# Optimization experiments

Measured on AMD Instinct MI355X. Metric: run time of the kernel, lower is better.

Reference implementation:

```python
import jax, jax.numpy as jnp
import numpy as np

V, E, H, D, DFF, NB, C, B, T = 32000, 512, 256, 512, 2048, 4, 16, 32, 512
PAD, BOS, EOS = 0, 1, 2


def positional_encoding(t, d):
    pos = jnp.arange(t, dtype=jnp.float32)[:, None]
    i = jnp.arange(0, d, 2, dtype=jnp.float32)
    div = jnp.exp(-(jnp.log(10000.0)) * i / d)
    pe = jnp.zeros((t, d), jnp.float32)
    pe = pe.at[:, 0::2].set(jnp.sin(pos * div))
    pe = pe.at[:, 1::2].set(jnp.cos(pos * div))
    return pe


def layernorm(x, g, b, eps=1e-5):
    mu = jnp.mean(x, -1, keepdims=True)
    var = jnp.mean((x - mu) ** 2, -1, keepdims=True)
    return (x - mu) * jax.lax.rsqrt(var + eps) * g + b


def gru_dir(xs, w_ih, w_hh, b_ih, b_hh, reverse):
    # xs: (B,T,E); precompute input projections for all t (one big GEMM)
    gi = jnp.einsum('bte,ge->btg', xs, w_ih) + b_ih  # (B,T,3H)
    h0 = jnp.zeros((xs.shape[0], H), xs.dtype)

    def step(h, gi_t):
        gh = h @ w_hh.T + b_hh
        i_r, i_z, i_n = jnp.split(gi_t, 3, -1)
        h_r, h_z, h_n = jnp.split(gh, 3, -1)
        r = jax.nn.sigmoid(i_r + h_r)
        z = jax.nn.sigmoid(i_z + h_z)
        n = jnp.tanh(i_n + r * h_n)
        h_new = (1.0 - z) * n + z * h
        return h_new, h_new

    _, hs = jax.lax.scan(step, h0, jnp.swapaxes(gi, 0, 1), reverse=reverse)
    return jnp.swapaxes(hs, 0, 1)  # (B,T,H)


def forward(x, y, embed_W, w_ih_f, w_hh_f, b_ih_f, b_hh_f, w_ih_b, w_hh_b, b_ih_b, b_hh_b,
            ff_w1, ff_b1, ff_w2, ff_b2, ln_g, ln_b, fc_w, fc_b, trans):
    h = embed_W[x]                                   # (B,T,E)
    h = h + positional_encoding(h.shape[1], E)[None]
    hf = gru_dir(h, w_ih_f, w_hh_f, b_ih_f, b_hh_f, False)
    hb = gru_dir(h, w_ih_b, w_hh_b, b_ih_b, b_hh_b, True)
    h = jnp.concatenate([hf, hb], -1)                # (B,T,D)
    for i in range(NB):                              # FeedForward blocks (residual + LN)
        ff = jax.nn.relu(h @ ff_w1[i] + ff_b1[i]) @ ff_w2[i] + ff_b2[i]
        h = layernorm(h + ff, ln_g[i], ln_b[i])
    logits = h @ fc_w + fc_b                         # (B,T,C) emissions

    # --- CRF viterbi decode ---
    mask = (y != PAD)                                # (B,T) bool
    emit = jnp.swapaxes(logits, 0, 1)                # (T,B,C)
    m = jnp.swapaxes(mask, 0, 1)                     # (T,B)
    score0 = trans[BOS][None] + emit[0]              # (B,C)

    def vstep(score, inp):
        e_t, m_t = inp                               # (B,C), (B,)
        cand = score[:, :, None] + trans[None] + e_t[:, None, :]  # (B,prev,cur)
        new = jnp.max(cand, axis=1)
        bp = jnp.argmax(cand, axis=1)                # (B,C)
        new = jnp.where(m_t[:, None], new, score)
        return new, bp

    final, bps = jax.lax.scan(vstep, score0, (emit[1:], m[1:]))  # bps: (T-1,B,C)
    final = final + trans[:, EOS][None]
    best_score = jnp.max(final, -1)                  # (B,)
    last_tag = jnp.argmax(final, -1)                 # (B,)

    def back(tag, inp):
        bp_t, m_t = inp
        prev = jnp.take_along_axis(bp_t, tag[:, None], axis=1)[:, 0]
        prev = jnp.where(m_t, prev, tag)
        return prev, tag

    first_tag, rest = jax.lax.scan(back, last_tag, (bps, m[1:]), reverse=True)
    path = jnp.swapaxes(jnp.concatenate([first_tag[None], rest], 0), 0, 1)  # (B,T)
    return best_score, path


def setup_inputs():
    key = jax.random.key(0)
    ks = jax.random.split(key, 16)
    nrm = lambda k, sh, sc: jax.random.normal(k, sh, jnp.float32) * sc
    s = 1.0 / float(np.sqrt(H))
    inp = {}
    inp['x'] = jax.random.randint(ks[0], (B, T), 1, V)
    inp['y'] = jax.random.randint(ks[1], (B, T), 0, 13) + 3  # in [3,16): no pad/bos/eos
    inp['embed_W'] = nrm(ks[2], (V, E), 0.02)
    inp['w_ih_f'] = nrm(ks[3], (3 * H, E), s); inp['w_hh_f'] = nrm(ks[4], (3 * H, H), s)
    inp['b_ih_f'] = nrm(ks[5], (3 * H,), s); inp['b_hh_f'] = nrm(ks[6], (3 * H,), s)
    inp['w_ih_b'] = nrm(ks[7], (3 * H, E), s); inp['w_hh_b'] = nrm(ks[8], (3 * H, H), s)
    inp['b_ih_b'] = nrm(ks[9], (3 * H,), s); inp['b_hh_b'] = nrm(ks[10], (3 * H,), s)
    inp['ff_w1'] = nrm(ks[11], (NB, D, DFF), 1.0 / float(np.sqrt(D)))
    inp['ff_b1'] = jnp.zeros((NB, DFF), jnp.float32)
    inp['ff_w2'] = nrm(ks[12], (NB, DFF, D), 1.0 / float(np.sqrt(DFF)))
    inp['ff_b2'] = jnp.zeros((NB, D), jnp.float32)
    inp['ln_g'] = jnp.ones((NB, D), jnp.float32); inp['ln_b'] = jnp.zeros((NB, D), jnp.float32)
    inp['fc_w'] = nrm(ks[13], (D, C), 1.0 / float(np.sqrt(D)))
    inp['fc_b'] = jnp.zeros((C,), jnp.float32)
    inp['trans'] = nrm(ks[14], (C, C), 0.1)
    return inp


def reference(x, y, embed_W, w_ih_f, w_hh_f, b_ih_f, b_hh_f, w_ih_b, w_hh_b, b_ih_b, b_hh_b,
              ff_w1, ff_b1, ff_w2, ff_b2, ln_g, ln_b, fc_w, fc_b, trans):
    return forward(x, y, embed_W, w_ih_f, w_hh_f, b_ih_f, b_hh_f, w_ih_b, w_hh_b, b_ih_b, b_hh_b,
                   ff_w1, ff_b1, ff_w2, ff_b2, ln_g, ln_b, fc_w, fc_b, trans)
```

## Files before the change

### kernel.cpp

```cpp
#include <hip/hip_runtime.h>

#define DEV __device__ __forceinline__

using short8 = __attribute__((ext_vector_type(8))) short;
using f32x4  = __attribute__((ext_vector_type(4))) float;

DEV float b2f(short s) {
  union { unsigned u; float f; } c;
  c.u = ((unsigned)(unsigned short)s) << 16;
  return c.f;
}
DEV short f2b(float f) {
  union { float f; unsigned u; } c; c.f = f;
  unsigned u = c.u + 0x7fffu + ((c.u >> 16) & 1u);
  return (short)(u >> 16);
}
DEV float fast_sigmoid(float x) {
  return __builtin_amdgcn_rcpf(1.f + __expf(-x));
}
DEV float fast_tanh(float x) {
  return 1.f - 2.f * __builtin_amdgcn_rcpf(1.f + __expf(2.f * x));
}
DEV void async_ld16(const void* g, void* lds) {
  __builtin_amdgcn_global_load_lds(
      (const __attribute__((address_space(1))) void*)(unsigned long long)g,
      (__attribute__((address_space(3))) void*)(unsigned)(unsigned long long)lds,
      16, 0, 0);
}

__global__ __launch_bounds__(256) void k_cvt2(const float* __restrict__ a, const float* __restrict__ b,
                                              short* __restrict__ oa, short* __restrict__ ob) {
  int blk = blockIdx.x;
  const float* in; short* out; int base;
  if (blk < 384) { in = a; out = oa; base = blk; }
  else           { in = b; out = ob; base = blk - 384; }
  int i = base * 256 + threadIdx.x;
  f32x4 v = *(const f32x4*)(in + (size_t)i * 4);
  short4 o;
#pragma unroll
  for (int j = 0; j < 4; j++) ((short*)&o)[j] = f2b(v[j]);
  *(short4*)(out + (size_t)i * 4) = o;
}

__global__ __launch_bounds__(256) void k_w8(const float* __restrict__ wf,
                                            const float* __restrict__ wb,
                                            long* __restrict__ out) {
  int flat = blockIdx.x * 256 + threadIdx.x;
  int lane = flat & 63;
  int r1 = flat >> 6;
  int kb = r1 & 7;
  int r2 = r1 >> 3;
  int g = r2 % 3;
  int r3 = r2 / 3;
  int v = r3 & 15;
  int d = r3 >> 4;
  const float* w = d ? wb : wf;
  int row = g * 256 + v * 16 + (lane & 15);
  int k0 = kb * 32 + (lane >> 4) * 8;
  const float* p = w + (size_t)row * 256 + k0;
  f32x4 f0 = *(const f32x4*)(p);
  f32x4 f1 = *(const f32x4*)(p + 4);
  int u0 = __builtin_amdgcn_cvt_pk_fp8_f32(f0[0], f0[1], 0, false);
  u0 = __builtin_amdgcn_cvt_pk_fp8_f32(f0[2], f0[3], u0, true);
  int u1 = __builtin_amdgcn_cvt_pk_fp8_f32(f1[0], f1[1], 0, false);
  u1 = __builtin_amdgcn_cvt_pk_fp8_f32(f1[2], f1[3], u1, true);
  out[flat] = ((long)(unsigned)u1 << 32) | (unsigned)u0;
}

__global__ __launch_bounds__(256) void k_embed(const int* __restrict__ x,
                                               const float* __restrict__ W,
                                               short* __restrict__ h0) {
  int flat = blockIdx.x * 256 + threadIdx.x;
  int row  = flat >> 6;
  int e0   = (flat & 63) << 3;
  int tok  = x[row];
  int t    = row & 511;
  const float* wp = W + (size_t)tok * 512 + e0;
  float v[8];
  *(f32x4*)v       = *(const f32x4*)(wp);
  *(f32x4*)(v + 4) = *(const f32x4*)(wp + 4);
  short8 o;
#pragma unroll
  for (int i = 0; i < 8; i += 2) {
    float f = expf(-9.210340371976184f * (float)(e0 + i) * (1.f / 512.f));
    float ang = (float)t * f;
    o[i]     = f2b(v[i]     + sinf(ang));
    o[i + 1] = f2b(v[i + 1] + cosf(ang));
  }
  *(short8*)(h0 + (size_t)flat * 8) = o;
}

__global__ __launch_bounds__(256) void k_transcvt(const float* __restrict__ in0,
                                                  short* __restrict__ out0, int R, int C) {
  __shared__ float tile[32][33];
  int mat = blockIdx.x >> 10;
  const float* in = in0 + (size_t)mat * 1048576;
  short* out = out0 + (size_t)mat * 1048576;
  int blk = blockIdx.x & 1023;
  int ct = C >> 5;
  int bc = blk % ct, br = blk / ct;
  int r0 = br << 5, c0 = bc << 5;
  for (int i = threadIdx.x; i < 1024; i += 256) {
    int r = i >> 5, c = i & 31;
    tile[r][c] = in[(size_t)(r0 + r) * C + c0 + c];
  }
  __syncthreads();
  for (int i = threadIdx.x; i < 1024; i += 256) {
    int c = i >> 5, r = i & 31;
    out[(size_t)(c0 + c) * R + r0 + r] = f2b(tile[r][c]);
  }
}

template <int MODE>
__global__ __launch_bounds__(256) void k_gemm(const short* __restrict__ A,
    const short* __restrict__ B, const float* __restrict__ bias,
    float* __restrict__ Cf, short* __restrict__ Cb, int M, int N, int K) {
  __shared__ short smA[8192];
  __shared__ short smB[8192];
  const int tid = threadIdx.x, lane = tid & 63, wave = tid >> 6;
  const int m15 = lane & 15, q8 = (lane >> 4) << 3;
  const int tn = N >> 7;
  const int bm = blockIdx.x / tn, bn = blockIdx.x % tn;
  const int wm = wave & 1, wn = wave >> 1;
  const f32x4 z4 = {0.f, 0.f, 0.f, 0.f};
  f32x4 acc[4][4];
#pragma unroll
  for (int i = 0; i < 4; i++)
#pragma unroll
    for (int j = 0; j < 4; j++) acc[i][j] = z4;

  for (int k0 = 0; k0 < K; k0 += 64) {
#pragma unroll
    for (int is = 0; is < 4; is++) {
      int c = is * 4 + wave;
      int mb = c & 7, kb = c >> 3;
      async_ld16(A + (size_t)(bm * 128 + mb * 16 + m15) * K + k0 + kb * 32 + q8, smA + c * 512);
      async_ld16(B + (size_t)(bn * 128 + mb * 16 + m15) * K + k0 + kb * 32 + q8, smB + c * 512);
    }
    __syncthreads();
#pragma unroll
    for (int kk = 0; kk < 2; kk++) {
      short8 af[4], bf[4];
#pragma unroll
      for (int i = 0; i < 4; i++)
        af[i] = *(const short8*)(smA + (kk * 8 + wm * 4 + i) * 512 + lane * 8);
#pragma unroll
      for (int j = 0; j < 4; j++)
        bf[j] = *(const short8*)(smB + (kk * 8 + wn * 4 + j) * 512 + lane * 8);
#pragma unroll
      for (int i = 0; i < 4; i++)
#pragma unroll
        for (int j = 0; j < 4; j++)
          acc[i][j] = __builtin_amdgcn_mfma_f32_16x16x32_bf16(af[i], bf[j], acc[i][j], 0, 0, 0);
    }
    __syncthreads();
  }
#pragma unroll
  for (int j = 0; j < 4; j++) {
    int col = bn * 128 + wn * 64 + j * 16 + m15;
    float bv = bias[col];
#pragma unroll
    for (int i = 0; i < 4; i++) {
      int row0 = bm * 128 + wm * 64 + i * 16 + ((lane >> 4) << 2);
#pragma unroll
      for (int r = 0; r < 4; r++) {
        float v = acc[i][j][r] + bv;
        int rr = row0 + r;
        if (MODE == 0) {
          Cf[(size_t)rr * N + col] = v;
        } else if (MODE == 1) {
          if (v < 0.f) v = 0.f;
          Cb[(size_t)rr * N + col] = f2b(v);
        } else {
          Cb[((size_t)((rr & 511) * 32 + (rr >> 9))) * 768 + col] = f2b(v);
        }
      }
    }
  }
}

__global__ __launch_bounds__(1024) void k_gru(
    const long* __restrict__ w8,
    const float* __restrict__ bhh_f, const float* __restrict__ bhh_b,
    const short* __restrict__ gi16_f, const short* __restrict__ gi16_b,
    short* __restrict__ hcat16) {
  __shared__ char  hb[2][4352];
  __shared__ float smG[16][200];
  const int blk = blockIdx.x;
  const int d = blk & 1, bg = blk >> 1;
  const int tid = threadIdx.x, lane = tid & 63, v = tid >> 6;
  const int m15 = lane & 15, quad = lane >> 4, q8 = quad * 8;
  const int col = v * 16 + m15;
  const int brow = quad;
  const float* bhh = d ? bhh_b : bhh_f;
  const short* gi  = d ? gi16_b : gi16_f;

  long Bf[3][8];
  {
    const long* wp = w8 + (size_t)(d * 16 + v) * 1536;
#pragma unroll
    for (int g = 0; g < 3; g++)
#pragma unroll
      for (int kb = 0; kb < 8; kb++)
        Bf[g][kb] = wp[(g * 8 + kb) * 64 + lane];
  }
  float bh[3];
#pragma unroll
  for (int g = 0; g < 3; g++) bh[g] = bhh[g * 256 + col];

  for (int i = tid; i < 2176; i += 1024) ((int*)hb)[i] = 0;

  const int t0 = d ? 511 : 0;
  const long gdelta = (long)(d ? -1 : 1) * 32 * 768;
  const long hdelta = (long)(d ? -1 : 1) * 32 * 512;
  const short* gp0 = gi + ((size_t)t0 * 32 + bg * 4 + brow) * 768 + col;
  const short* gp1 = gp0 + 256;
  const short* gp2 = gp0 + 512;
  short* hflush = hcat16 + ((size_t)t0 * 32 + bg * 4 + brow) * 512 + d * 256 + col;

  float gic0 = b2f(*gp0), gic1 = b2f(*gp1), gic2 = b2f(*gp2);
  gp0 += gdelta; gp1 += gdelta; gp2 += gdelta;
  float hprev = 0.f;
  unsigned obuf[4] = {0u, 0u, 0u, 0u};
  const f32x4 z4 = {0.f, 0.f, 0.f, 0.f};
  __syncthreads();

  for (int s = 0; s < 512; s++) {
    short n0 = 0, n1 = 0, n2 = 0;
    if (s < 511) {
      n0 = *gp0; n1 = *gp1; n2 = *gp2;
      gp0 += gdelta; gp1 += gdelta; gp2 += gdelta;
    }
    const char* hs = hb[s & 1];
    f32x4 acc0 = z4, acc1 = z4, acc2 = z4;
#pragma unroll
    for (int kb = 0; kb < 8; kb++) {
      long a = *(const long*)(hs + m15 * 272 + kb * 32 + q8);
      acc0 = __builtin_amdgcn_mfma_f32_16x16x32_fp8_fp8(a, Bf[0][kb], acc0, 0, 0, 0);
      acc1 = __builtin_amdgcn_mfma_f32_16x16x32_fp8_fp8(a, Bf[1][kb], acc1, 0, 0, 0);
      acc2 = __builtin_amdgcn_mfma_f32_16x16x32_fp8_fp8(a, Bf[2][kb], acc2, 0, 0, 0);
    }
    if (quad == 0) {
#pragma unroll
      for (int i = 0; i < 4; i++) {
        smG[v][i * 16 + m15]       = acc0[i];
        smG[v][64 + i * 16 + m15]  = acc1[i];
        smG[v][128 + i * 16 + m15] = acc2[i];
      }
    }
    float gr = smG[v][lane];
    float gz = smG[v][64 + lane];
    float gn = smG[v][128 + lane];
    float r = fast_sigmoid(gic0 + gr + bh[0]);
    float z = fast_sigmoid(gic1 + gz + bh[1]);
    float n = fast_tanh(gic2 + r * (gn + bh[2]));
    float h = (1.f - z) * n + z * hprev;
    hprev = h;
    int p8 = __builtin_amdgcn_cvt_pk_fp8_f32(h, h, 0, false);
    hb[(s + 1) & 1][brow * 272 + col] = (char)(p8 & 0xff);
    unsigned hb16 = (unsigned)(unsigned short)f2b(h);
    int idx = s & 7;
    if ((idx & 1) == 0) obuf[idx >> 1] = hb16;
    else                obuf[idx >> 1] |= hb16 << 16;
    if (idx == 7) {
      short* p = hflush;
#pragma unroll
      for (int k = 0; k < 8; k++) {
        *p = (short)(obuf[k >> 1] >> ((k & 1) * 16));
        p += hdelta;
      }
      hflush += 8 * hdelta;
    }
    gic0 = b2f(n0); gic1 = b2f(n1); gic2 = b2f(n2);
    __syncthreads();
  }
}

template <int FIRST>
__global__ __launch_bounds__(256) void k_ln(const float* __restrict__ hinf,
    const float* __restrict__ ff, const float* __restrict__ gw,
    const float* __restrict__ bw, float* __restrict__ hout, short* __restrict__ h16) {
  int row = blockIdx.x * 4 + (threadIdx.x >> 6);
  int lane = threadIdx.x & 63;
  size_t base = (size_t)row * 512 + lane * 8;
  f32x4 x0, x1;
  if (FIRST) {
    short8 hv = *(const short8*)(h16 + base);
#pragma unroll
    for (int i = 0; i < 4; i++) { x0[i] = b2f(hv[i]); x1[i] = b2f(hv[4 + i]); }
  } else {
    x0 = *(const f32x4*)(hinf + base);
    x1 = *(const f32x4*)(hinf + base + 4);
  }
  f32x4 y0 = *(const f32x4*)(ff + base);
  f32x4 y1 = *(const f32x4*)(ff + base + 4);
  x0 += y0; x1 += y1;
  float s = x0[0] + x0[1] + x0[2] + x0[3] + x1[0] + x1[1] + x1[2] + x1[3];
#pragma unroll
  for (int off = 32; off >= 1; off >>= 1) s += __shfl_xor(s, off);
  float mu = s * (1.f / 512.f);
  float vv = 0.f;
#pragma unroll
  for (int i = 0; i < 4; i++) { float d0 = x0[i] - mu, d1 = x1[i] - mu; vv += d0 * d0 + d1 * d1; }
#pragma unroll
  for (int off = 32; off >= 1; off >>= 1) vv += __shfl_xor(vv, off);
  float rs = rsqrtf(vv * (1.f / 512.f) + 1e-5f);
  int e = lane * 8;
  f32x4 g0 = *(const f32x4*)(gw + e), g1 = *(const f32x4*)(gw + e + 4);
  f32x4 bb0 = *(const f32x4*)(bw + e), bb1 = *(const f32x4*)(bw + e + 4);
  f32x4 o0, o1; short8 ob;
#pragma unroll
  for (int i = 0; i < 4; i++) {
    float a = (x0[i] - mu) * rs * g0[i] + bb0[i];
    float b = (x1[i] - mu) * rs * g1[i] + bb1[i];
    o0[i] = a; o1[i] = b; ob[i] = f2b(a); ob[4 + i] = f2b(b);
  }
  *(f32x4*)(hout + base) = o0;
  *(f32x4*)(hout + base + 4) = o1;
  *(short8*)(h16 + base) = ob;
}

__global__ __launch_bounds__(256) void k_fc(const float* __restrict__ h,
    const float* __restrict__ fcw, const float* __restrict__ bias,
    float* __restrict__ logits) {
  int row = blockIdx.x * 4 + (threadIdx.x >> 6);
  int lane = threadIdx.x & 63;
  int c = lane & 15, part = lane >> 4;
  const float* ph = h + (size_t)row * 512 + part * 128;
  const float* pw = fcw + (size_t)part * 128 * 16 + c;
  float acc = 0.f;
#pragma unroll 8
  for (int k = 0; k < 128; k += 4) {
    f32x4 hv = *(const f32x4*)(ph + k);
    acc += hv[0] * pw[(k) * 16] + hv[1] * pw[(k + 1) * 16]
         + hv[2] * pw[(k + 2) * 16] + hv[3] * pw[(k + 3) * 16];
  }
  acc += __shfl_xor(acc, 16);
  acc += __shfl_xor(acc, 32);
  if (part == 0) logits[(size_t)row * 16 + c] = acc + bias[c];
}

__global__ __launch_bounds__(64) void k_crf(const float* __restrict__ logits,
    const int* __restrict__ y, const float* __restrict__ trans,
    float* __restrict__ out) {
  __shared__ float tr[16][16];
  __shared__ unsigned char bp[511][16];
  int b = blockIdx.x, lane = threadIdx.x;
  for (int i = lane; i < 256; i += 64) tr[i >> 4][i & 15] = trans[i];
  __syncthreads();
  int cur = lane & 15;
  const float* lg = logits + (size_t)b * 16;
  const int* yb = y + b * 512;
  float score = tr[1][cur] + lg[cur];
  float e_next = lg[512 + cur];
  int y_next = yb[1];
  for (int t = 1; t < 512; t++) {
    float e = e_next; int ym = y_next;
    if (t < 511) { e_next = lg[(t + 1) * 512 + cur]; y_next = yb[t + 1]; }
    float best = -3.4e38f; int arg = 0;
#pragma unroll
    for (int p = 0; p < 16; p++) {
      float cand = __shfl(score, p) + tr[p][cur];
      if (cand > best) { best = cand; arg = p; }
    }
    if (lane < 16) bp[t - 1][cur] = (unsigned char)arg;
    float ns = best + e;
    if (ym == 0) ns = score;
    score = ns;
  }
  score += tr[cur][2];
  float best = -3.4e38f; int argb = 0;
#pragma unroll
  for (int p = 0; p < 16; p++) {
    float sp = __shfl(score, p);
    if (sp > best) { best = sp; argb = p; }
  }
  __syncthreads();
  if (lane == 0) {
    out[b] = best;
    float* po = out + 32 + (size_t)b * 512;
    int tag = argb;
    po[511] = (float)tag;
    for (int t = 511; t >= 1; t--) {
      int prev = bp[t - 1][tag];
      if (yb[t] == 0) prev = tag;
      po[t - 1] = (float)prev;
      tag = prev;
    }
  }
}

extern "C" void kernel_launch(void* const* d_in, const int* in_sizes, int n_in,
                              void* d_out, int out_size, void* d_ws, size_t ws_size,
                              hipStream_t stream) {
  const int*   x      = (const int*)d_in[0];
  const int*   y      = (const int*)d_in[1];
  const float* embedW = (const float*)d_in[2];
  const float* w_ih_f = (const float*)d_in[3];
  const float* w_hh_f = (const float*)d_in[4];
  const float* b_ih_f = (const float*)d_in[5];
  const float* b_hh_f = (const float*)d_in[6];
  const float* w_ih_b = (const float*)d_in[7];
  const float* w_hh_b = (const float*)d_in[8];
  const float* b_ih_b = (const float*)d_in[9];
  const float* b_hh_b = (const float*)d_in[10];
  const float* ff_w1  = (const float*)d_in[11];
  const float* ff_b1  = (const float*)d_in[12];
  const float* ff_w2  = (const float*)d_in[13];
  const float* ff_b2  = (const float*)d_in[14];
  const float* ln_g   = (const float*)d_in[15];
  const float* ln_b   = (const float*)d_in[16];
  const float* fc_w   = (const float*)d_in[17];
  const float* fc_b   = (const float*)d_in[18];
  const float* trans  = (const float*)d_in[19];
  float* out = (float*)d_out;

  char* ws = (char*)d_ws;
  short* h0     = (short*)(ws + 0);
  short* gi16_f = (short*)(ws + 16777216);
  short* gi16_b = (short*)(ws + 41943040);
  short* mid    = (short*)(ws + 16777216);
  float* ffout  = (float*)(ws + 83886080);
  short* wihf16 = (short*)(ws + 117440512);
  short* wihb16 = (short*)(ws + 118226944);
  long*  w8     = (long*) (ws + 119013376);
  short* w1t    = (short*)(ws + 119799808);
  short* w2t    = (short*)(ws + 128188416);
  short* hcat16 = (short*)(ws + 136577024);
  float* hres   = (float*)(ws + 153354240);
  float* logits = (float*)(ws + 186908672);

  k_embed<<<4096, 256, 0, stream>>>(x, embedW, h0);
  k_cvt2<<<768, 256, 0, stream>>>(w_ih_f, w_ih_b, wihf16, wihb16);
  k_w8<<<192, 256, 0, stream>>>(w_hh_f, w_hh_b, w8);
  k_transcvt<<<4096, 256, 0, stream>>>(ff_w1, w1t, 512, 2048);
  k_transcvt<<<4096, 256, 0, stream>>>(ff_w2, w2t, 2048, 512);

  k_gemm<2><<<768, 256, 0, stream>>>(h0, wihf16, b_ih_f, nullptr, gi16_f, 16384, 768, 512);
  k_gemm<2><<<768, 256, 0, stream>>>(h0, wihb16, b_ih_b, nullptr, gi16_b, 16384, 768, 512);

  k_gru<<<16, 1024, 0, stream>>>(w8, b_hh_f, b_hh_b, gi16_f, gi16_b, hcat16);

  for (int i = 0; i < 4; i++) {
    k_gemm<1><<<2048, 256, 0, stream>>>(hcat16, w1t + (size_t)i * 1048576, ff_b1 + i * 2048,
                                        nullptr, mid, 16384, 2048, 512);
    k_gemm<0><<<512, 256, 0, stream>>>(mid, w2t + (size_t)i * 1048576, ff_b2 + i * 512,
                                       ffout, nullptr, 16384, 512, 2048);
    if (i == 0)
      k_ln<1><<<4096, 256, 0, stream>>>(nullptr, ffout, ln_g, ln_b, hres, hcat16);
    else
      k_ln<0><<<4096, 256, 0, stream>>>(hres, ffout, ln_g + i * 512, ln_b + i * 512, hres, hcat16);
  }
  k_fc<<<4096, 256, 0, stream>>>(hres, fc_w, fc_b, logits);
  k_crf<<<32, 64, 0, stream>>>(logits, y, trans, out);
}
```

Baseline: 1.779 ms.

## Merge GRU input GEMMs and swizzle GRU hidden-state LDS layout for vector loads

The forward and backward input-projection GEMMs become one N=1536 GEMM that writes an interleaved gate buffer. This relies on the two bf16 weight copies sitting next to each other in the workspace, and a new bias2 argument selects the bias per half. In the serial GRU kernel, the fp8 hidden state is stored in a permuted, XOR-swizzled LDS layout. Each lane can then fetch all eight MFMA A fragments with four 128-bit loads instead of eight 64-bit loads, cutting LDS latency on the recurrent critical path. The bf16 output flush also moves to the top of the next step so its stores overlap that step's work.

```diff
diff --git a/kernel.cpp b/kernel.cpp
--- a/kernel.cpp
+++ b/kernel.cpp
@@ -4,6 +4,7 @@
 
 using short8 = __attribute__((ext_vector_type(8))) short;
 using f32x4  = __attribute__((ext_vector_type(4))) float;
+using i64x2  = __attribute__((ext_vector_type(2))) long;
 
 DEV float b2f(short s) {
   union { unsigned u; float f; } c;
@@ -114,6 +115,7 @@
 template <int MODE>
 __global__ __launch_bounds__(256) void k_gemm(const short* __restrict__ A,
     const short* __restrict__ B, const float* __restrict__ bias,
+    const float* __restrict__ bias2,
     float* __restrict__ Cf, short* __restrict__ Cb, int M, int N, int K) {
   __shared__ short smA[8192];
   __shared__ short smB[8192];
@@ -158,7 +160,9 @@
 #pragma unroll
   for (int j = 0; j < 4; j++) {
     int col = bn * 128 + wn * 64 + j * 16 + m15;
-    float bv = bias[col];
+    float bv;
+    if (MODE == 3) bv = (col < 768) ? bias[col] : bias2[col - 768];
+    else           bv = bias[col];
 #pragma unroll
     for (int i = 0; i < 4; i++) {
       int row0 = bm * 128 + wm * 64 + i * 16 + ((lane >> 4) << 2);
@@ -172,7 +176,7 @@
           if (v < 0.f) v = 0.f;
           Cb[(size_t)rr * N + col] = f2b(v);
         } else {
-          Cb[((size_t)((rr & 511) * 32 + (rr >> 9))) * 768 + col] = f2b(v);
+          Cb[((size_t)((rr & 511) * 32 + (rr >> 9))) * 1536 + col] = f2b(v);
         }
       }
     }
@@ -182,18 +186,17 @@
 __global__ __launch_bounds__(1024) void k_gru(
     const long* __restrict__ w8,
     const float* __restrict__ bhh_f, const float* __restrict__ bhh_b,
-    const short* __restrict__ gi16_f, const short* __restrict__ gi16_b,
+    const short* __restrict__ gi16,
     short* __restrict__ hcat16) {
-  __shared__ char  hb[2][4352];
+  __shared__ __align__(16) char hb[2][4096];
   __shared__ float smG[16][200];
   const int blk = blockIdx.x;
   const int d = blk & 1, bg = blk >> 1;
   const int tid = threadIdx.x, lane = tid & 63, v = tid >> 6;
-  const int m15 = lane & 15, quad = lane >> 4, q8 = quad * 8;
+  const int m15 = lane & 15, quad = lane >> 4;
   const int col = v * 16 + m15;
   const int brow = quad;
   const float* bhh = d ? bhh_b : bhh_f;
-  const short* gi  = d ? gi16_b : gi16_f;
 
   long Bf[3][8];
   {
@@ -208,12 +211,20 @@
 #pragma unroll
   for (int g = 0; g < 3; g++) bh[g] = bhh[g * 256 + col];
 
-  for (int i = tid; i < 2176; i += 1024) ((int*)hb)[i] = 0;
+  const int sw = (m15 & 3) << 4;
+  const int aof0 = m15 * 256 + ((quad * 64 +  0) ^ sw);
+  const int aof1 = m15 * 256 + ((quad * 64 + 16) ^ sw);
+  const int aof2 = m15 * 256 + ((quad * 64 + 32) ^ sw);
+  const int aof3 = m15 * 256 + ((quad * 64 + 48) ^ sw);
+  const int Lw = (((col >> 3) & 3) << 6) + ((col >> 5) << 3) + (col & 7);
+  const int wofs = brow * 256 + (Lw ^ (brow << 4));
+
+  for (int i = tid; i < 2048; i += 1024) ((int*)hb)[i] = 0;
 
   const int t0 = d ? 511 : 0;
-  const long gdelta = (long)(d ? -1 : 1) * 32 * 768;
+  const long gdelta = (long)(d ? -1 : 1) * 32 * 1536;
   const long hdelta = (long)(d ? -1 : 1) * 32 * 512;
-  const short* gp0 = gi + ((size_t)t0 * 32 + bg * 4 + brow) * 768 + col;
+  const short* gp0 = gi16 + ((size_t)t0 * 32 + bg * 4 + brow) * 1536 + d * 768 + col;
   const short* gp1 = gp0 + 256;
   const short* gp2 = gp0 + 512;
   short* hflush = hcat16 + ((size_t)t0 * 32 + bg * 4 + brow) * 512 + d * 256 + col;
@@ -226,19 +237,32 @@
   __syncthreads();
 
   for (int s = 0; s < 512; s++) {
+    if ((s & 7) == 0 && s) {
+      short* p = hflush;
+#pragma unroll
+      for (int k = 0; k < 8; k++) {
+        *p = (short)(obuf[k >> 1] >> ((k & 1) * 16));
+        p += hdelta;
+      }
+      hflush += 8 * hdelta;
+    }
     short n0 = 0, n1 = 0, n2 = 0;
     if (s < 511) {
       n0 = *gp0; n1 = *gp1; n2 = *gp2;
       gp0 += gdelta; gp1 += gdelta; gp2 += gdelta;
     }
     const char* hs = hb[s & 1];
+    i64x2 p0 = *(const i64x2*)(hs + aof0);
+    i64x2 p1 = *(const i64x2*)(hs + aof1);
+    i64x2 p2 = *(const i64x2*)(hs + aof2);
+    i64x2 p3 = *(const i64x2*)(hs + aof3);
+    long Af[8] = {p0[0], p0[1], p1[0], p1[1], p2[0], p2[1], p3[0], p3[1]};
     f32x4 acc0 = z4, acc1 = z4, acc2 = z4;
 #pragma unroll
     for (int kb = 0; kb < 8; kb++) {
-      long a = *(const long*)(hs + m15 * 272 + kb * 32 + q8);
-      acc0 = __builtin_amdgcn_mfma_f32_16x16x32_fp8_fp8(a, Bf[0][kb], acc0, 0, 0, 0);
-      acc1 = __builtin_amdgcn_mfma_f32_16x16x32_fp8_fp8(a, Bf[1][kb], acc1, 0, 0, 0);
-      acc2 = __builtin_amdgcn_mfma_f32_16x16x32_fp8_fp8(a, Bf[2][kb], acc2, 0, 0, 0);
+      acc0 = __builtin_amdgcn_mfma_f32_16x16x32_fp8_fp8(Af[kb], Bf[0][kb], acc0, 0, 0, 0);
+      acc1 = __builtin_amdgcn_mfma_f32_16x16x32_fp8_fp8(Af[kb], Bf[1][kb], acc1, 0, 0, 0);
+      acc2 = __builtin_amdgcn_mfma_f32_16x16x32_fp8_fp8(Af[kb], Bf[2][kb], acc2, 0, 0, 0);
     }
     if (quad == 0) {
 #pragma unroll
@@ -257,22 +281,21 @@
     float h = (1.f - z) * n + z * hprev;
     hprev = h;
     int p8 = __builtin_amdgcn_cvt_pk_fp8_f32(h, h, 0, false);
-    hb[(s + 1) & 1][brow * 272 + col] = (char)(p8 & 0xff);
+    hb[(s + 1) & 1][wofs] = (char)(p8 & 0xff);
     unsigned hb16 = (unsigned)(unsigned short)f2b(h);
     int idx = s & 7;
     if ((idx & 1) == 0) obuf[idx >> 1] = hb16;
     else                obuf[idx >> 1] |= hb16 << 16;
-    if (idx == 7) {
-      short* p = hflush;
-#pragma unroll
-      for (int k = 0; k < 8; k++) {
-        *p = (short)(obuf[k >> 1] >> ((k & 1) * 16));
-        p += hdelta;
-      }
-      hflush += 8 * hdelta;
-    }
     gic0 = b2f(n0); gic1 = b2f(n1); gic2 = b2f(n2);
     __syncthreads();
+  }
+  {
+    short* p = hflush;
+#pragma unroll
+    for (int k = 0; k < 8; k++) {
+      *p = (short)(obuf[k >> 1] >> ((k & 1) * 16));
+      p += hdelta;
+    }
   }
 }
 
@@ -417,8 +440,7 @@
 
   char* ws = (char*)d_ws;
   short* h0     = (short*)(ws + 0);
-  short* gi16_f = (short*)(ws + 16777216);
-  short* gi16_b = (short*)(ws + 41943040);
+  short* gi16   = (short*)(ws + 16777216);
   short* mid    = (short*)(ws + 16777216);
   float* ffout  = (float*)(ws + 83886080);
   short* wihf16 = (short*)(ws + 117440512);
@@ -436,16 +458,15 @@
   k_transcvt<<<4096, 256, 0, stream>>>(ff_w1, w1t, 512, 2048);
   k_transcvt<<<4096, 256, 0, stream>>>(ff_w2, w2t, 2048, 512);
 
-  k_gemm<2><<<768, 256, 0, stream>>>(h0, wihf16, b_ih_f, nullptr, gi16_f, 16384, 768, 512);
-  k_gemm<2><<<768, 256, 0, stream>>>(h0, wihb16, b_ih_b, nullptr, gi16_b, 16384, 768, 512);
-
-  k_gru<<<16, 1024, 0, stream>>>(w8, b_hh_f, b_hh_b, gi16_f, gi16_b, hcat16);
+  k_gemm<3><<<1536, 256, 0, stream>>>(h0, wihf16, b_ih_f, b_ih_b, nullptr, gi16, 16384, 1536, 512);
+
+  k_gru<<<16, 1024, 0, stream>>>(w8, b_hh_f, b_hh_b, gi16, hcat16);
 
   for (int i = 0; i < 4; i++) {
     k_gemm<1><<<2048, 256, 0, stream>>>(hcat16, w1t + (size_t)i * 1048576, ff_b1 + i * 2048,
-                                        nullptr, mid, 16384, 2048, 512);
+                                        nullptr, nullptr, mid, 16384, 2048, 512);
     k_gemm<0><<<512, 256, 0, stream>>>(mid, w2t + (size_t)i * 1048576, ff_b2 + i * 512,
-                                       ffout, nullptr, 16384, 512, 2048);
+                                       nullptr, ffout, nullptr, 16384, 512, 2048);
     if (i == 0)
       k_ln<1><<<4096, 256, 0, stream>>>(nullptr, ffout, ln_g, ln_b, hres, hcat16);
     else
```

Measured after the change: 1.768 ms. Within noise of the previous version (-0.6%).
